# Performance work log

Hardware: AMD Instinct MI355X
Metric: run time of the kernel (lower is better)

## Reference

```python
import jax, jax.numpy as jnp
import numpy as np

N_NODES = 50000
DIM = 128
N_EDGES = 800000
N_UID = 4096
ORDER = 3
LN_EPS = 1e-5


def setup_inputs() -> dict:
    key = jax.random.key(0)
    ks = jax.random.split(key, 6)
    scale = 1.0 / np.sqrt(DIM)
    embedding = jax.random.normal(ks[0], (N_NODES, DIM), jnp.float32) * np.sqrt(2.0 / DIM)  # kaiming-ish
    W = jax.random.normal(ks[1], (ORDER, DIM, DIM), jnp.float32) * scale
    b = jnp.zeros((ORDER, DIM), jnp.float32)
    gamma = jnp.ones((ORDER, DIM), jnp.float32)
    beta = jnp.zeros((ORDER, DIM), jnp.float32)
    src = jax.random.randint(ks[2], (N_EDGES,), 0, N_NODES, jnp.int32)
    dst = jax.random.randint(ks[3], (N_EDGES,), 0, N_NODES, jnp.int32)
    uid = jax.random.randint(ks[4], (N_UID,), 0, N_NODES, jnp.int32)
    return {"embedding": embedding, "W": W, "b": b, "gamma": gamma,
            "beta": beta, "src": src, "dst": dst, "uid": uid}


def _layer_norm(x, g, bta):
    mu = jnp.mean(x, axis=-1, keepdims=True)
    var = jnp.var(x, axis=-1, keepdims=True)
    return (x - mu) * jax.lax.rsqrt(var + LN_EPS) * g + bta


def reference(embedding, W, b, gamma, beta, src, dst, uid):
    # in-degree per destination node (DGL 'gcn' aggregator uses in_degrees)
    deg = jax.ops.segment_sum(jnp.ones((src.shape[0],), embedding.dtype), dst,
                              num_segments=N_NODES)  # [N]
    inv = (1.0 / (deg + 1.0))[:, None]  # [N,1]
    feats = embedding
    for i in range(ORDER):
        # gather source features, scatter-sum into destinations
        neigh = jax.ops.segment_sum(feats[src], dst, num_segments=N_NODES)  # [N,D]
        h = (neigh + feats) * inv                    # gcn-style mean incl. self
        h = jnp.einsum('nd,ed->ne', h, W[i]) + b[i]  # fc_neigh
        feats = jax.nn.elu(_layer_norm(h, gamma[i], beta[i]))
    return feats[uid]  # [N_UID, D]
```

## Files before the change

### kernel.cpp

```cpp
#include <hip/hip_runtime.h>
#include <math.h>

typedef unsigned int   uint;
typedef unsigned short ushort;
typedef unsigned char  uchar;

#define N_NODES 50000
#define DIM     128
#define N_EDGES 800000
#define N_UID   4096
#define LN_EPS  1e-5f
#define RST     132
#define XST     136
#define BSH     6
#define BND     64
#define NBUCK   782
#define BCAP    1280
#define PCHUNK  2048
#define NCHUNK  ((N_EDGES + PCHUNK - 1) / PCHUNK)
#define QBLK    (N_NODES / 16)
#define WBLK    48
#define MROW    50004

typedef __attribute__((ext_vector_type(8))) short bf16x8;
typedef __attribute__((ext_vector_type(4))) float f32x4;
typedef __attribute__((ext_vector_type(4))) uint  u32x4;

__device__ __forceinline__ uint pack_bf16(float a, float b) {
    uint ua = __builtin_bit_cast(uint, a);
    uint ub = __builtin_bit_cast(uint, b);
    uint ra = (ua + 0x7fffu + ((ua >> 16) & 1u)) >> 16;
    uint rb = (ub + 0x7fffu + ((ub >> 16) & 1u)) >> 16;
    return ra | (rb << 16);
}

__global__ __launch_bounds__(256) void prep_kernel(const float* __restrict__ emb,
                                                   uchar* __restrict__ Q0, float2* __restrict__ M0,
                                                   const float* __restrict__ W, ushort* __restrict__ WB,
                                                   int* __restrict__ bcur,
                                                   float2* __restrict__ M1, float2* __restrict__ M2) {
    const int t = threadIdx.x, b = blockIdx.x;
    if (b < QBLK) {
        const int row = b * 16 + (t >> 4);
        const int seg = t & 15;
        const float* rp = emb + (size_t)row * DIM + seg * 8;
        const float4 v0 = ((const float4*)rp)[0];
        const float4 v1 = ((const float4*)rp)[1];
        float vs[8] = {v0.x, v0.y, v0.z, v0.w, v1.x, v1.y, v1.z, v1.w};
        float mn = vs[0], mx = vs[0];
        #pragma unroll
        for (int j = 1; j < 8; ++j) { mn = fminf(mn, vs[j]); mx = fmaxf(mx, vs[j]); }
        #pragma unroll
        for (int m = 1; m < 16; m <<= 1) {
            mn = fminf(mn, __shfl_xor(mn, m));
            mx = fmaxf(mx, __shfl_xor(mx, m));
        }
        const float rng = mx - mn;
        const float rcp = (rng > 0.0f) ? 255.0f / rng : 0.0f;
        uint bq[8];
        #pragma unroll
        for (int j = 0; j < 8; ++j)
            bq[j] = (uint)fminf(255.0f, fmaf(vs[j] - mn, rcp, 0.5f));
        uint2 q;
        q.x = bq[0] | (bq[1] << 8) | (bq[2] << 16) | (bq[3] << 24);
        q.y = bq[4] | (bq[5] << 8) | (bq[6] << 16) | (bq[7] << 24);
        ((uint2*)(Q0 + (size_t)row * DIM))[seg] = q;
        if (seg == 0) M0[row] = make_float2(rng * (1.0f / 255.0f), mn);
    } else if (b < QBLK + WBLK) {
        const int i = (b - QBLK) * 256 + t;
        const float4 v = ((const float4*)W)[i];
        uint2 p;
        p.x = pack_bf16(v.x, v.y);
        p.y = pack_bf16(v.z, v.w);
        ((uint2*)WB)[i] = p;
    } else {
        for (int i = t; i < NBUCK; i += 256) bcur[i] = 0;
        if (t == 0) {
            M0[N_NODES] = make_float2(0.0f, 0.0f);
            M1[N_NODES] = make_float2(0.0f, 0.0f);
            M2[N_NODES] = make_float2(0.0f, 0.0f);
        }
    }
}

__global__ __launch_bounds__(256) void part_kernel(const int* __restrict__ src, const int* __restrict__ dst,
                                                   int* __restrict__ bcur, int* __restrict__ pak) {
    __shared__ int h[NBUCK];
    __shared__ int base[NBUCK];
    __shared__ int cur[NBUCK];
    const int t  = threadIdx.x;
    const int e0 = blockIdx.x * PCHUNK;
    const int e1 = min(e0 + PCHUNK, N_EDGES);
    for (int i = t; i < NBUCK; i += 256) h[i] = 0;
    __syncthreads();
    for (int i = e0 + t; i < e1; i += 256)
        atomicAdd(&h[dst[i] >> BSH], 1);
    __syncthreads();
    for (int i = t; i < NBUCK; i += 256) {
        if (h[i]) base[i] = atomicAdd(&bcur[i], h[i]);
        cur[i] = 0;
    }
    __syncthreads();
    for (int i = e0 + t; i < e1; i += 256) {
        const int s = src[i], d = dst[i];
        const int b = d >> BSH;
        const int q = base[b] + atomicAdd(&cur[b], 1);
        if (q < BCAP)
            pak[b * BCAP + q] = (s << BSH) | (d & (BND - 1));
    }
}

__global__ __launch_bounds__(256) void bucket_kernel(const int* __restrict__ pak, const int* __restrict__ bcur,
                                                     int* __restrict__ off, int* __restrict__ degv,
                                                     int* __restrict__ csr) {
    __shared__ int cnt[BND];
    __shared__ int pos[BND];
    const int b = blockIdx.x, t = threadIdx.x;
    const int e0 = b * BCAP;
    const int m  = min(bcur[b], BCAP);
    if (t < BND) cnt[t] = 0;
    __syncthreads();
    for (int i = t; i < m; i += 256) atomicAdd(&cnt[pak[e0 + i] & (BND - 1)], 1);
    __syncthreads();
    const int v = (t < BND) ? cnt[t] : 0;
    if (t < BND) pos[t] = v;
    __syncthreads();
    for (int o = 1; o < BND; o <<= 1) {
        int x = 0;
        if (t < BND && t >= o) x = pos[t - o];
        __syncthreads();
        if (t < BND) pos[t] += x;
        __syncthreads();
    }
    const int excl = (t < BND) ? (pos[t] - v) : 0;
    const int node = b * BND + t;
    if (t < BND && node < N_NODES) { off[node] = e0 + excl; degv[node] = v; }
    __syncthreads();
    if (t < BND) pos[t] = excl;
    __syncthreads();
    for (int i = t; i < m; i += 256) {
        const int p = pak[e0 + i];
        const int q = atomicAdd(&pos[p & (BND - 1)], 1);
        csr[e0 + q] = p >> BSH;
    }
}

template <int NT, bool OUT_FP32>
__global__ __launch_bounds__(NT, 4) void layer_kernel(
    const uchar* __restrict__ qin, const float2* __restrict__ meta_in,
    uchar* __restrict__ qout, float2* __restrict__ meta_out, float* __restrict__ fpout,
    const int* __restrict__ off, const int* __restrict__ degv,
    const int* __restrict__ csr, const int* __restrict__ uidmap,
    const ushort* __restrict__ wb, const float* __restrict__ bias,
    const float* __restrict__ gamma, const float* __restrict__ beta, int nrows)
{
    constexpr int NRT = NT / 16;
    __shared__ ushort xs[NRT * XST];
    __shared__ float  ys[NRT * RST];
    const int t = threadIdx.x;
    const int rows = blockIdx.x * NRT;

    {
        const int lx   = t & 15;
        const int st   = t >> 4;
        const int slot = rows + st;
        const bool valid = slot < nrows;
        int n = 0;
        if (valid) n = uidmap ? uidmap[slot] : slot;
        const int d0 = off[n];
        const int deg = valid ? degv[n] : 0;
        const int total = deg + 1;

        float a[8] = {0,0,0,0,0,0,0,0};
        float O = 0.0f;
        const int rounds = (total + 7) >> 3;
        int id[8], idn[8];
        uint2 qv[8];
        float2 mt[8];

#define LIDS(ID, BASE) { _Pragma("unroll") for (int k = 0; k < 8; ++k) {        \
            const int pos = (BASE) + k;                                         \
            const int c = csr[d0 + ((pos > 0) ? pos - 1 : 0)];                  \
            ID[k] = (pos == 0) ? n : ((pos < total) ? c : N_NODES); } }

        LIDS(id, 0);
        for (int r = 0; r < rounds; ++r) {
            #pragma unroll
            for (int k = 0; k < 8; ++k) {
                qv[k] = ((const uint2*)(qin + (size_t)id[k] * DIM))[lx];
                mt[k] = meta_in[id[k]];
            }
            const bool more = (r + 1 < rounds);
            if (more) LIDS(idn, (r + 1) * 8);
            #pragma unroll
            for (int k = 0; k < 8; ++k) {
                const float s = mt[k].x;
                const uint x0 = qv[k].x, x1 = qv[k].y;
                a[0] = fmaf((float)(x0 & 0xffu),         s, a[0]);
                a[1] = fmaf((float)((x0 >> 8) & 0xffu),  s, a[1]);
                a[2] = fmaf((float)((x0 >> 16) & 0xffu), s, a[2]);
                a[3] = fmaf((float)(x0 >> 24),           s, a[3]);
                a[4] = fmaf((float)(x1 & 0xffu),         s, a[4]);
                a[5] = fmaf((float)((x1 >> 8) & 0xffu),  s, a[5]);
                a[6] = fmaf((float)((x1 >> 16) & 0xffu), s, a[6]);
                a[7] = fmaf((float)(x1 >> 24),           s, a[7]);
                O += mt[k].y;
            }
            if (more) {
                #pragma unroll
                for (int k = 0; k < 8; ++k) id[k] = idn[k];
            }
        }
#undef LIDS

        const float iv = 1.0f / (float)total;
        uint4 p;
        p.x = pack_bf16((a[0] + O) * iv, (a[1] + O) * iv);
        p.y = pack_bf16((a[2] + O) * iv, (a[3] + O) * iv);
        p.z = pack_bf16((a[4] + O) * iv, (a[5] + O) * iv);
        p.w = pack_bf16((a[6] + O) * iv, (a[7] + O) * iv);
        *((uint4*)(xs + st * XST + lx * 8)) = p;
    }
    __syncthreads();

    {
        const int wave = t >> 6, lane = t & 63;
        int row_off, col_off;
        if constexpr (NT == 512) { row_off = (wave >> 2) * 16; col_off = (wave & 3) * 32; }
        else                     { row_off = 0;                col_off = wave * 32; }
        const int lm   = lane & 15;
        const int quad = lane >> 4;
        f32x4 acc[2] = {f32x4{0,0,0,0}, f32x4{0,0,0,0}};
        const ushort* xrow = xs + (row_off + lm) * XST + quad * 8;
        const ushort* __restrict__ wrow = wb + (size_t)(col_off + lm) * DIM + quad * 8;
        #pragma unroll
        for (int kk = 0; kk < 4; ++kk) {
            const bf16x8 af = __builtin_bit_cast(bf16x8, *(const u32x4*)(xrow + kk * 32));
            #pragma unroll
            for (int c = 0; c < 2; ++c) {
                const bf16x8 bfr = __builtin_bit_cast(bf16x8,
                    *(const u32x4*)(wrow + (size_t)c * 16 * DIM + kk * 32));
                acc[c] = __builtin_amdgcn_mfma_f32_16x16x32_bf16(af, bfr, acc[c], 0, 0, 0);
            }
        }
        #pragma unroll
        for (int c = 0; c < 2; ++c) {
            #pragma unroll
            for (int r = 0; r < 4; ++r)
                ys[(row_off + quad * 4 + r) * RST + col_off + c * 16 + lm] = acc[c][r];
        }
    }
    __syncthreads();

    {
        const int r   = t >> 4;
        const int seg = t & 15;
        const int db  = seg * 8;
        const float* yr = ys + r * RST + db;
        float vs[8];
        {
            const float4 y0 = ((const float4*)yr)[0];
            const float4 y1 = ((const float4*)yr)[1];
            const float4 b0 = ((const float4*)(bias + db))[0];
            const float4 b1 = ((const float4*)(bias + db))[1];
            vs[0] = y0.x + b0.x; vs[1] = y0.y + b0.y; vs[2] = y0.z + b0.z; vs[3] = y0.w + b0.w;
            vs[4] = y1.x + b1.x; vs[5] = y1.y + b1.y; vs[6] = y1.z + b1.z; vs[7] = y1.w + b1.w;
        }
        float s1 = 0.0f, s2 = 0.0f;
        #pragma unroll
        for (int i = 0; i < 8; ++i) { s1 += vs[i]; s2 += vs[i] * vs[i]; }
        #pragma unroll
        for (int m = 1; m < 16; m <<= 1) {
            s1 += __shfl_xor(s1, m);
            s2 += __shfl_xor(s2, m);
        }
        const float mu  = s1 * (1.0f / 128.0f);
        const float var = s2 * (1.0f / 128.0f) - mu * mu;
        const float rs  = rsqrtf(var + LN_EPS);
        float ov[8];
        {
            const float4 g0 = ((const float4*)(gamma + db))[0];
            const float4 g1 = ((const float4*)(gamma + db))[1];
            const float4 t0 = ((const float4*)(beta + db))[0];
            const float4 t1 = ((const float4*)(beta + db))[1];
            float z;
            z = (vs[0] - mu) * rs * g0.x + t0.x; ov[0] = (z > 0.0f) ? z : __expf(z) - 1.0f;
            z = (vs[1] - mu) * rs * g0.y + t0.y; ov[1] = (z > 0.0f) ? z : __expf(z) - 1.0f;
            z = (vs[2] - mu) * rs * g0.z + t0.z; ov[2] = (z > 0.0f) ? z : __expf(z) - 1.0f;
            z = (vs[3] - mu) * rs * g0.w + t0.w; ov[3] = (z > 0.0f) ? z : __expf(z) - 1.0f;
            z = (vs[4] - mu) * rs * g1.x + t1.x; ov[4] = (z > 0.0f) ? z : __expf(z) - 1.0f;
            z = (vs[5] - mu) * rs * g1.y + t1.y; ov[5] = (z > 0.0f) ? z : __expf(z) - 1.0f;
            z = (vs[6] - mu) * rs * g1.z + t1.z; ov[6] = (z > 0.0f) ? z : __expf(z) - 1.0f;
            z = (vs[7] - mu) * rs * g1.w + t1.w; ov[7] = (z > 0.0f) ? z : __expf(z) - 1.0f;
        }
        const int slot = rows + r;
        if (OUT_FP32) {
            if (slot < nrows) {
                float* op = fpout + (size_t)slot * DIM + db;
                ((float4*)op)[0] = make_float4(ov[0], ov[1], ov[2], ov[3]);
                ((float4*)op)[1] = make_float4(ov[4], ov[5], ov[6], ov[7]);
            }
        } else {
            float mn = ov[0], mx = ov[0];
            #pragma unroll
            for (int j = 1; j < 8; ++j) { mn = fminf(mn, ov[j]); mx = fmaxf(mx, ov[j]); }
            #pragma unroll
            for (int m = 1; m < 16; m <<= 1) {
                mn = fminf(mn, __shfl_xor(mn, m));
                mx = fmaxf(mx, __shfl_xor(mx, m));
            }
            if (slot < nrows) {
                const float rng = mx - mn;
                const float rcp = (rng > 0.0f) ? 255.0f / rng : 0.0f;
                uint bq[8];
                #pragma unroll
                for (int j = 0; j < 8; ++j)
                    bq[j] = (uint)fminf(255.0f, fmaf(ov[j] - mn, rcp, 0.5f));
                uint2 q;
                q.x = bq[0] | (bq[1] << 8) | (bq[2] << 16) | (bq[3] << 24);
                q.y = bq[4] | (bq[5] << 8) | (bq[6] << 16) | (bq[7] << 24);
                ((uint2*)(qout + (size_t)slot * DIM))[seg] = q;
                if (seg == 0) meta_out[slot] = make_float2(rng * (1.0f / 255.0f), mn);
            }
        }
    }
}

extern "C" void kernel_launch(void* const* d_in, const int* in_sizes, int n_in,
                              void* d_out, int out_size, void* d_ws, size_t ws_size,
                              hipStream_t stream) {
    const float* emb   = (const float*)d_in[0];
    const float* W     = (const float*)d_in[1];
    const float* bias  = (const float*)d_in[2];
    const float* gamma = (const float*)d_in[3];
    const float* beta  = (const float*)d_in[4];
    const int*   src   = (const int*)d_in[5];
    const int*   dst   = (const int*)d_in[6];
    const int*   uid   = (const int*)d_in[7];

    const size_t QSZ = (size_t)(N_NODES + 1) * DIM;
    uchar*  Q0  = (uchar*)d_ws;
    uchar*  Q1  = Q0 + QSZ;
    uchar*  Q2  = Q1 + QSZ;
    ushort* WB  = (ushort*)(Q2 + QSZ);
    float2* M0  = (float2*)(WB + 3 * DIM * DIM);
    float2* M1  = M0 + MROW;
    float2* M2  = M1 + MROW;
    int*    off  = (int*)(M2 + MROW);
    int*    degv = off + (N_NODES + 4);
    int*    bcur = degv + (N_NODES + 4);
    int*    pak  = bcur + (NBUCK + 2);
    int*    csr  = pak + NBUCK * BCAP;

    prep_kernel<<<QBLK + WBLK + 1, 256, 0, stream>>>(emb, Q0, M0, W, WB, bcur, M1, M2);
    part_kernel<<<NCHUNK, 256, 0, stream>>>(src, dst, bcur, pak);
    bucket_kernel<<<NBUCK, 256, 0, stream>>>(pak, bcur, off, degv, csr);

    layer_kernel<512, false><<<(N_NODES + 31) / 32, 512, 0, stream>>>(
        Q0, M0, Q1, M1, nullptr, off, degv, csr, nullptr, WB,
        bias, gamma, beta, N_NODES);
    layer_kernel<256, false><<<(N_NODES + 15) / 16, 256, 0, stream>>>(
        Q1, M1, Q2, M2, nullptr, off, degv, csr, nullptr, WB + DIM * DIM,
        bias + DIM, gamma + DIM, beta + DIM, N_NODES);
    layer_kernel<512, true><<<N_UID / 32, 512, 0, stream>>>(
        Q2, M2, nullptr, nullptr, (float*)d_out, off, degv, csr, uid,
        WB + 2 * DIM * DIM, bias + 2 * DIM, gamma + 2 * DIM, beta + 2 * DIM, N_UID);
}
```

Baseline: 203.7 us.

## Share quantization scale per 32-row group and cache metadata in LDS

```diff
diff --git a/kernel.cpp b/kernel.cpp
--- a/kernel.cpp
+++ b/kernel.cpp
@@ -18,9 +18,9 @@
 #define BCAP    1280
 #define PCHUNK  2048
 #define NCHUNK  ((N_EDGES + PCHUNK - 1) / PCHUNK)
-#define QBLK    (N_NODES / 16)
-#define WBLK    48
-#define MROW    50004
+#define PGRP    1563
+#define PADID   (PGRP * 32)
+#define QROWS   (PADID + 32)
 
 typedef __attribute__((ext_vector_type(8))) short bf16x8;
 typedef __attribute__((ext_vector_type(4))) float f32x4;
@@ -34,51 +34,65 @@
     return ra | (rb << 16);
 }
 
-__global__ __launch_bounds__(256) void prep_kernel(const float* __restrict__ emb,
-                                                   uchar* __restrict__ Q0, float2* __restrict__ M0,
+__global__ __launch_bounds__(512) void prep_kernel(const float* __restrict__ emb,
+                                                   uchar* __restrict__ Q0, float2* __restrict__ MG0,
                                                    const float* __restrict__ W, ushort* __restrict__ WB,
                                                    int* __restrict__ bcur,
-                                                   float2* __restrict__ M1, float2* __restrict__ M2) {
+                                                   float2* __restrict__ MG1, float2* __restrict__ MG2) {
     const int t = threadIdx.x, b = blockIdx.x;
-    if (b < QBLK) {
-        const int row = b * 16 + (t >> 4);
+    if (b < PGRP) {
+        __shared__ float smn[32], smx[32];
+        const int row = b * 32 + (t >> 4);
         const int seg = t & 15;
-        const float* rp = emb + (size_t)row * DIM + seg * 8;
-        const float4 v0 = ((const float4*)rp)[0];
-        const float4 v1 = ((const float4*)rp)[1];
-        float vs[8] = {v0.x, v0.y, v0.z, v0.w, v1.x, v1.y, v1.z, v1.w};
-        float mn = vs[0], mx = vs[0];
-        #pragma unroll
-        for (int j = 1; j < 8; ++j) { mn = fminf(mn, vs[j]); mx = fmaxf(mx, vs[j]); }
+        const bool valid = row < N_NODES;
+        float vs[8];
+        float mn = 3.4e38f, mx = -3.4e38f;
+        if (valid) {
+            const float* rp = emb + (size_t)row * DIM + seg * 8;
+            const float4 v0 = ((const float4*)rp)[0];
+            const float4 v1 = ((const float4*)rp)[1];
+            vs[0]=v0.x; vs[1]=v0.y; vs[2]=v0.z; vs[3]=v0.w;
+            vs[4]=v1.x; vs[5]=v1.y; vs[6]=v1.z; vs[7]=v1.w;
+            mn = vs[0]; mx = vs[0];
+            #pragma unroll
+            for (int j = 1; j < 8; ++j) { mn = fminf(mn, vs[j]); mx = fmaxf(mx, vs[j]); }
+        }
         #pragma unroll
         for (int m = 1; m < 16; m <<= 1) {
             mn = fminf(mn, __shfl_xor(mn, m));
             mx = fmaxf(mx, __shfl_xor(mx, m));
         }
-        const float rng = mx - mn;
+        if (seg == 0) { smn[t >> 4] = mn; smx[t >> 4] = mx; }
+        __syncthreads();
+        float gmn = smn[0], gmx = smx[0];
+        #pragma unroll
+        for (int i = 1; i < 32; ++i) { gmn = fminf(gmn, smn[i]); gmx = fmaxf(gmx, smx[i]); }
+        const float rng = gmx - gmn;
         const float rcp = (rng > 0.0f) ? 255.0f / rng : 0.0f;
-        uint bq[8];
-        #pragma unroll
-        for (int j = 0; j < 8; ++j)
-            bq[j] = (uint)fminf(255.0f, fmaf(vs[j] - mn, rcp, 0.5f));
-        uint2 q;
-        q.x = bq[0] | (bq[1] << 8) | (bq[2] << 16) | (bq[3] << 24);
-        q.y = bq[4] | (bq[5] << 8) | (bq[6] << 16) | (bq[7] << 24);
-        ((uint2*)(Q0 + (size_t)row * DIM))[seg] = q;
-        if (seg == 0) M0[row] = make_float2(rng * (1.0f / 255.0f), mn);
-    } else if (b < QBLK + WBLK) {
-        const int i = (b - QBLK) * 256 + t;
+        if (valid) {
+            uint bq[8];
+            #pragma unroll
+            for (int j = 0; j < 8; ++j)
+                bq[j] = (uint)fminf(255.0f, fmaf(vs[j] - gmn, rcp, 0.5f));
+            uint2 q;
+            q.x = bq[0] | (bq[1] << 8) | (bq[2] << 16) | (bq[3] << 24);
+            q.y = bq[4] | (bq[5] << 8) | (bq[6] << 16) | (bq[7] << 24);
+            ((uint2*)(Q0 + (size_t)row * DIM))[seg] = q;
+        }
+        if (t == 0) MG0[b] = make_float2(rng * (1.0f / 255.0f), gmn);
+    } else if (b < PGRP + 24) {
+        const int i = (b - PGRP) * 512 + t;
         const float4 v = ((const float4*)W)[i];
         uint2 p;
         p.x = pack_bf16(v.x, v.y);
         p.y = pack_bf16(v.z, v.w);
         ((uint2*)WB)[i] = p;
     } else {
-        for (int i = t; i < NBUCK; i += 256) bcur[i] = 0;
+        for (int i = t; i < NBUCK; i += 512) bcur[i] = 0;
         if (t == 0) {
-            M0[N_NODES] = make_float2(0.0f, 0.0f);
-            M1[N_NODES] = make_float2(0.0f, 0.0f);
-            M2[N_NODES] = make_float2(0.0f, 0.0f);
+            MG0[PGRP] = make_float2(0.0f, 0.0f);
+            MG1[PGRP] = make_float2(0.0f, 0.0f);
+            MG2[PGRP] = make_float2(0.0f, 0.0f);
         }
     }
 }
@@ -145,20 +159,24 @@
     }
 }
 
-template <int NT, bool OUT_FP32>
-__global__ __launch_bounds__(NT, 4) void layer_kernel(
-    const uchar* __restrict__ qin, const float2* __restrict__ meta_in,
-    uchar* __restrict__ qout, float2* __restrict__ meta_out, float* __restrict__ fpout,
+template <bool OUT_FP32>
+__global__ __launch_bounds__(512, 4) void layer_kernel(
+    const uchar* __restrict__ qin, const float2* __restrict__ mgin,
+    uchar* __restrict__ qout, float2* __restrict__ mgout, float* __restrict__ fpout,
     const int* __restrict__ off, const int* __restrict__ degv,
     const int* __restrict__ csr, const int* __restrict__ uidmap,
     const ushort* __restrict__ wb, const float* __restrict__ bias,
     const float* __restrict__ gamma, const float* __restrict__ beta, int nrows)
 {
-    constexpr int NRT = NT / 16;
-    __shared__ ushort xs[NRT * XST];
-    __shared__ float  ys[NRT * RST];
+    __shared__ ushort xs[32 * XST];
+    __shared__ float  ys[32 * RST];
+    __shared__ float2 metal[PGRP + 1];
+    __shared__ float  rmn[32], rmx[32];
     const int t = threadIdx.x;
-    const int rows = blockIdx.x * NRT;
+    const int rows = blockIdx.x * 32;
+
+    for (int i = t; i < PGRP + 1; i += 512) metal[i] = mgin[i];
+    __syncthreads();
 
     {
         const int lx   = t & 15;
@@ -176,25 +194,23 @@
         const int rounds = (total + 7) >> 3;
         int id[8], idn[8];
         uint2 qv[8];
-        float2 mt[8];
 
 #define LIDS(ID, BASE) { _Pragma("unroll") for (int k = 0; k < 8; ++k) {        \
             const int pos = (BASE) + k;                                         \
             const int c = csr[d0 + ((pos > 0) ? pos - 1 : 0)];                  \
-            ID[k] = (pos == 0) ? n : ((pos < total) ? c : N_NODES); } }
+            ID[k] = (pos == 0) ? n : ((pos < total) ? c : PADID); } }
 
         LIDS(id, 0);
         for (int r = 0; r < rounds; ++r) {
             #pragma unroll
-            for (int k = 0; k < 8; ++k) {
+            for (int k = 0; k < 8; ++k)
                 qv[k] = ((const uint2*)(qin + (size_t)id[k] * DIM))[lx];
-                mt[k] = meta_in[id[k]];
-            }
             const bool more = (r + 1 < rounds);
             if (more) LIDS(idn, (r + 1) * 8);
             #pragma unroll
             for (int k = 0; k < 8; ++k) {
-                const float s = mt[k].x;
+                const float2 mv = metal[id[k] >> 5];
+                const float s = mv.x;
                 const uint x0 = qv[k].x, x1 = qv[k].y;
                 a[0] = fmaf((float)(x0 & 0xffu),         s, a[0]);
                 a[1] = fmaf((float)((x0 >> 8) & 0xffu),  s, a[1]);
@@ -204,7 +220,7 @@
                 a[5] = fmaf((float)((x1 >> 8) & 0xffu),  s, a[5]);
                 a[6] = fmaf((float)((x1 >> 16) & 0xffu), s, a[6]);
                 a[7] = fmaf((float)(x1 >> 24),           s, a[7]);
-                O += mt[k].y;
+                O += mv.y;
             }
             if (more) {
                 #pragma unroll
@@ -225,9 +241,8 @@
 
     {
         const int wave = t >> 6, lane = t & 63;
-        int row_off, col_off;
-        if constexpr (NT == 512) { row_off = (wave >> 2) * 16; col_off = (wave & 3) * 32; }
-        else                     { row_off = 0;                col_off = wave * 32; }
+        const int row_off = (wave >> 2) * 16;
+        const int col_off = (wave & 3) * 32;
         const int lm   = lane & 15;
         const int quad = lane >> 4;
         f32x4 acc[2] = {f32x4{0,0,0,0}, f32x4{0,0,0,0}};
@@ -301,27 +316,36 @@
                 ((float4*)op)[1] = make_float4(ov[4], ov[5], ov[6], ov[7]);
             }
         } else {
-            float mn = ov[0], mx = ov[0];
-            #pragma unroll
-            for (int j = 1; j < 8; ++j) { mn = fminf(mn, ov[j]); mx = fmaxf(mx, ov[j]); }
+            const bool valid = slot < nrows;
+            float mn = valid ? ov[0] : 3.4e38f;
+            float mx = valid ? ov[0] : -3.4e38f;
+            if (valid) {
+                #pragma unroll
+                for (int j = 1; j < 8; ++j) { mn = fminf(mn, ov[j]); mx = fmaxf(mx, ov[j]); }
+            }
             #pragma unroll
             for (int m = 1; m < 16; m <<= 1) {
                 mn = fminf(mn, __shfl_xor(mn, m));
                 mx = fmaxf(mx, __shfl_xor(mx, m));
             }
-            if (slot < nrows) {
-                const float rng = mx - mn;
-                const float rcp = (rng > 0.0f) ? 255.0f / rng : 0.0f;
+            if (seg == 0) { rmn[r] = mn; rmx[r] = mx; }
+            __syncthreads();
+            float gmn = rmn[0], gmx = rmx[0];
+            #pragma unroll
+            for (int i = 1; i < 32; ++i) { gmn = fminf(gmn, rmn[i]); gmx = fmaxf(gmx, rmx[i]); }
+            const float rng = gmx - gmn;
+            const float rcp = (rng > 0.0f) ? 255.0f / rng : 0.0f;
+            if (valid) {
                 uint bq[8];
                 #pragma unroll
                 for (int j = 0; j < 8; ++j)
-                    bq[j] = (uint)fminf(255.0f, fmaf(ov[j] - mn, rcp, 0.5f));
+                    bq[j] = (uint)fminf(255.0f, fmaf(ov[j] - gmn, rcp, 0.5f));
                 uint2 q;
                 q.x = bq[0] | (bq[1] << 8) | (bq[2] << 16) | (bq[3] << 24);
                 q.y = bq[4] | (bq[5] << 8) | (bq[6] << 16) | (bq[7] << 24);
                 ((uint2*)(qout + (size_t)slot * DIM))[seg] = q;
-                if (seg == 0) meta_out[slot] = make_float2(rng * (1.0f / 255.0f), mn);
-            }
+            }
+            if (t == 0) mgout[blockIdx.x] = make_float2(rng * (1.0f / 255.0f), gmn);
         }
     }
 }
@@ -338,31 +362,34 @@
     const int*   dst   = (const int*)d_in[6];
     const int*   uid   = (const int*)d_in[7];
 
-    const size_t QSZ = (size_t)(N_NODES + 1) * DIM;
+    const size_t QSZ = (size_t)QROWS * DIM;
     uchar*  Q0  = (uchar*)d_ws;
     uchar*  Q1  = Q0 + QSZ;
     uchar*  Q2  = Q1 + QSZ;
     ushort* WB  = (ushort*)(Q2 + QSZ);
-    float2* M0  = (float2*)(WB + 3 * DIM * DIM);
-    float2* M1  = M0 + MROW;
-    float2* M2  = M1 + MROW;
-    int*    off  = (int*)(M2 + MROW);
+    float2* MG0 = (float2*)(WB + 3 * DIM * DIM);
+    float2* MG1 = MG0 + 1568;
+    float2* MG2 = MG1 + 1568;
+    int*    off  = (int*)(MG2 + 1568);
     int*    degv = off + (N_NODES + 4);
     int*    bcur = degv + (N_NODES + 4);
     int*    pak  = bcur + (NBUCK + 2);
     int*    csr  = pak + NBUCK * BCAP;
 
-    prep_kernel<<<QBLK + WBLK + 1, 256, 0, stream>>>(emb, Q0, M0, W, WB, bcur, M1, M2);
+    prep_kernel<<<PGRP + 24 + 1, 512, 0, stream>>>(emb, Q0, MG0, W, WB, bcur, MG1, MG2);
     part_kernel<<<NCHUNK, 256, 0, stream>>>(src, dst, bcur, pak);
     bucket_kernel<<<NBUCK, 256, 0, stream>>>(pak, bcur, off, degv, csr);
 
-    layer_kernel<512, false><<<(N_NODES + 31) / 32, 512, 0, stream>>>(
-        Q0, M0, Q1, M1, nullptr, off, degv, csr, nullptr, WB,
-        bias, gamma, beta, N_NODES);
-    layer_kernel<256, false><<<(N_NODES + 15) / 16, 256, 0, stream>>>(
-        Q1, M1, Q2, M2, nullptr, off, degv, csr, nullptr, WB + DIM * DIM,
-        bias + DIM, gamma + DIM, beta + DIM, N_NODES);
-    layer_kernel<512, true><<<N_UID / 32, 512, 0, stream>>>(
-        Q2, M2, nullptr, nullptr, (float*)d_out, off, degv, csr, uid,
-        WB + 2 * DIM * DIM, bias + 2 * DIM, gamma + 2 * DIM, beta + 2 * DIM, N_UID);
-}
+    const int lblk = (N_NODES + 31) / 32;
+
+    layer_kernel<false><<<lblk, 512, 0, stream>>>(Q0, MG0, Q1, MG1, nullptr,
+                                                  off, degv, csr, nullptr, WB,
+                                                  bias, gamma, beta, N_NODES);
+    layer_kernel<false><<<lblk, 512, 0, stream>>>(Q1, MG1, Q2, MG2, nullptr,
+                                                  off, degv, csr, nullptr, WB + DIM * DIM,
+                                                  bias + DIM, gamma + DIM, beta + DIM, N_NODES);
+    layer_kernel<true><<<N_UID / 32, 512, 0, stream>>>(Q2, MG2, nullptr, nullptr, (float*)d_out,
+                                                       off, degv, csr, uid, WB + 2 * DIM * DIM,
+                                                       bias + 2 * DIM, gamma + 2 * DIM,
+                                                       beta + 2 * DIM, N_UID);
+}
```

Result: slower. 207.9 us (+2.1%).
